# Kernel tuning notes

Hardware: AMD Instinct MI355X
Metric: run time of the kernel (lower is better)

## Reference

```python
import jax, jax.numpy as jnp
import numpy as np

EMBED_DIM = 768
HEAD_DIM = 64
BATCH = 8
SEQ = 4096


def setup_inputs() -> dict:
    key = jax.random.key(0)
    k_x, k_q, k_k, k_v = jax.random.split(key, 4)
    input_ids = jax.random.normal(k_x, (BATCH, SEQ, EMBED_DIM), dtype=jnp.float32)
    # nn.Linear(embed, head, bias=False): weight shape [head, embed]; y = x @ W.T
    scale = 1.0 / np.sqrt(EMBED_DIM)
    Wq = jax.random.normal(k_q, (HEAD_DIM, EMBED_DIM), dtype=jnp.float32) * scale
    Wk = jax.random.normal(k_k, (HEAD_DIM, EMBED_DIM), dtype=jnp.float32) * scale
    Wv = jax.random.normal(k_v, (HEAD_DIM, EMBED_DIM), dtype=jnp.float32) * scale
    return {"input_ids": input_ids, "Wq": Wq, "Wk": Wk, "Wv": Wv}


def reference(input_ids, Wq, Wk, Wv):
    # Projections. NOTE: the original module (faithfully reproduced) computes
    # v with q_net, so Wv is unused in the forward math.
    q = jnp.einsum('bse,he->bsh', input_ids, Wq)  # [B,S,H]
    k = jnp.einsum('bse,he->bsh', input_ids, Wk)  # [B,S,H]
    v = jnp.einsum('bse,he->bsh', input_ids, Wq)  # bug in source: uses q_net
    seq_len = q.shape[1]
    # Non-standard scaling: divide by sqrt(seq_len), not sqrt(head_dim)
    scores = jnp.einsum('bqh,bkh->bqk', q, k) / jnp.sqrt(jnp.float32(seq_len))
    # Non-standard softmax axis: over the query axis (dim=1)
    attn_weights = jax.nn.softmax(scores, axis=1)  # [B,Sq,Sk]
    return jnp.einsum('bqk,bkh->bqh', attn_weights, v)
```

## Files before the change

### kernel.cpp

```cpp
#include <hip/hip_runtime.h>
#include <hip/hip_bf16.h>
#include <cstdint>


#define BATCH 8
#define SEQ   4096
#define EMB   768
#define HD    64
#define NROW  (BATCH*SEQ)

#define QSCALE 0.1803368801111201f
#define KSCALE 0.125f
#define CSCALE 5.545177444479562f

typedef float  f32x4  __attribute__((ext_vector_type(4)));
typedef float  f32x16 __attribute__((ext_vector_type(16)));
typedef __bf16 bf16x8 __attribute__((ext_vector_type(8)));
typedef unsigned short u16x8_t __attribute__((ext_vector_type(8)));
typedef unsigned int   u32x4_t __attribute__((ext_vector_type(4)));

__device__ __forceinline__ f32x4 mfma16(bf16x8 a, bf16x8 b, f32x4 c) {
  return __builtin_amdgcn_mfma_f32_16x16x32_bf16(a, b, c, 0, 0, 0);
}
__device__ __forceinline__ f32x16 mfma32(bf16x8 a, bf16x8 b, f32x16 c) {
  return __builtin_amdgcn_mfma_f32_32x32x16_bf16(a, b, c, 0, 0, 0);
}
__device__ __forceinline__ unsigned short f2b(float f) {
  __bf16 h = (__bf16)f;
  return __builtin_bit_cast(unsigned short, h);
}
__device__ __forceinline__ float b2f(unsigned short u) {
  unsigned int x = ((unsigned int)u) << 16;
  return __builtin_bit_cast(float, x);
}
__device__ __forceinline__ unsigned short f2h(float f) {
  _Float16 h = (_Float16)f;
  return __builtin_bit_cast(unsigned short, h);
}
__device__ __forceinline__ float h2f(unsigned short u) {
  return (float)__builtin_bit_cast(_Float16, u);
}
__device__ __forceinline__ bf16x8 ldsA(const unsigned short* p) {
  return __builtin_bit_cast(bf16x8, *(const u16x8_t*)p);
}
__device__ __forceinline__ bf16x8 ldg8(const unsigned short* p) {
  return __builtin_bit_cast(bf16x8, *(const u16x8_t*)p);
}
__device__ __forceinline__ float expf2(float x) {
  float r; asm("v_exp_f32 %0, %1" : "=v"(r) : "v"(x)); return r;
}
__device__ __forceinline__ unsigned cvtpk(float lo, float hi) {
  unsigned r; asm("v_cvt_pk_bf16_f32 %0, %1, %2" : "=v"(r) : "v"(lo), "v"(hi)); return r;
}
__device__ __forceinline__ void plane32swap(unsigned &a, unsigned &b) {
  asm volatile("v_permlane32_swap_b32 %0, %1" : "+v"(a), "+v"(b));
}
__device__ __forceinline__ void glld16(const void* g, void* l) {
  __builtin_amdgcn_global_load_lds(
      (const __attribute__((address_space(1))) void*)g,
      (__attribute__((address_space(3))) void*)l, 16, 0, 0);
}
__device__ __forceinline__ int sidx(int r, int h) {
  return r * 64 + (h ^ ((r & 7) << 3));
}

__global__ __launch_bounds__(256) void wcvt_kernel(
    const float* __restrict__ Wq, const float* __restrict__ Wk,
    unsigned short* __restrict__ Wb) {
  int ci = blockIdx.x * 256 + threadIdx.x;
  int r = ci / 96, c8 = ci % 96;
  const float* src = (r < 64 ? Wq + (size_t)r * EMB : Wk + (size_t)(r - 64) * EMB) + c8 * 8;
  float4 a = *(const float4*)src, d = *(const float4*)(src + 4);
  u16x8_t o;
  o[0]=f2b(a.x); o[1]=f2b(a.y); o[2]=f2b(a.z); o[3]=f2b(a.w);
  o[4]=f2b(d.x); o[5]=f2b(d.y); o[6]=f2b(d.z); o[7]=f2b(d.w);
  *(u16x8_t*)(Wb + (size_t)ci * 8) = o;
}

__global__ __launch_bounds__(256) void proj_kernel(
    const float* __restrict__ X, const unsigned short* __restrict__ Wb,
    unsigned short* __restrict__ Qb, unsigned short* __restrict__ Kb) {
  __shared__ unsigned short Ws[2][8192];
  const int t = threadIdx.x, lane = t & 63, w = t >> 6;
  const int c = lane & 15, g = lane >> 4;
  const int row0 = blockIdx.x * 64;
  f32x4 acc[8];
#pragma unroll
  for (int f = 0; f < 8; ++f) { acc[f][0]=0.f; acc[f][1]=0.f; acc[f][2]=0.f; acc[f][3]=0.f; }

  auto STAGE = [&](int ec, int bb) {
#pragma unroll
    for (int i = 0; i < 4; ++i) {
      int rr = w + 4 * i;
      int ci = rr * 64 + lane;
      int r = ci >> 3, cL = ci & 7;
      glld16(Wb + (size_t)r * EMB + ec * 64 + (cL ^ (r & 7)) * 8, (void*)&Ws[bb][rr * 512]);
    }
  };
  const float* xrow = X + (size_t)(row0 + 16 * w + c) * EMB + 8 * g;
  float4 Xa[4], Xb[4];
  auto LOADX = [&](float4* R, int ec) {
    const float* xp = xrow + ec * 64;
    R[0] = *(const float4*)xp;        R[1] = *(const float4*)(xp + 4);
    R[2] = *(const float4*)(xp + 32); R[3] = *(const float4*)(xp + 36);
  };
  auto COMPUTE = [&](const float4* R, const unsigned short* Wt) {
    bf16x8 Af[2];
#pragma unroll
    for (int es = 0; es < 2; ++es) {
      float4 v0 = R[2 * es], v1 = R[2 * es + 1];
      u16x8_t tmp;
      tmp[0]=f2b(v0.x); tmp[1]=f2b(v0.y); tmp[2]=f2b(v0.z); tmp[3]=f2b(v0.w);
      tmp[4]=f2b(v1.x); tmp[5]=f2b(v1.y); tmp[6]=f2b(v1.z); tmp[7]=f2b(v1.w);
      Af[es] = __builtin_bit_cast(bf16x8, tmp);
    }
#pragma unroll
    for (int es = 0; es < 2; ++es)
#pragma unroll
      for (int f = 0; f < 8; ++f) {
        bf16x8 Bf = ldsA(&Wt[sidx(16 * f + c, es * 32 + 8 * g)]);
        acc[f] = mfma16(Af[es], Bf, acc[f]);
      }
  };

  LOADX(Xa, 0);
  STAGE(0, 0);
  __syncthreads();
#pragma unroll 1
  for (int e2 = 0; e2 < 6; ++e2) {
    int ec = 2 * e2;
    if (ec + 1 < 12) { STAGE(ec + 1, (ec + 1) & 1); LOADX(Xb, ec + 1); }
    COMPUTE(Xa, Ws[ec & 1]);
    __syncthreads();
    if (ec + 2 < 12) { STAGE(ec + 2, (ec + 2) & 1); LOADX(Xa, ec + 2); }
    COMPUTE(Xb, Ws[(ec + 1) & 1]);
    __syncthreads();
  }
#pragma unroll
  for (int f = 0; f < 8; ++f) {
    int n = 16 * f + c;
    float sc = (n < 64) ? QSCALE : KSCALE;
#pragma unroll
    for (int r = 0; r < 4; ++r) {
      int ROW = row0 + 16 * w + 4 * g + r;
      unsigned short bv = f2b(acc[f][r] * sc);
      if (n < 64) Qb[(size_t)ROW * 64 + n] = bv;
      else        Kb[(size_t)ROW * 64 + (n - 64)] = bv;
    }
  }
}

__global__ __launch_bounds__(256) void colsum_kernel(
    const unsigned short* __restrict__ Qb, const unsigned short* __restrict__ Kb,
    float* __restrict__ Zpart) {
  __shared__ unsigned short Qs[2][8192];
  const int t = threadIdx.x, lane = t & 63, w = t >> 6;
  const int c = lane & 31, hi = lane >> 5;
  const int fid = blockIdx.x;
  const int b = fid & 7, rem = fid >> 3;
  const int kt = rem & 15, qs = rem >> 4;
  const size_t kbase = (size_t)b * SEQ + kt * 256;
  const size_t qbase0 = (size_t)b * SEQ + qs * 1024;

  bf16x8 Kf[2][4];
#pragma unroll
  for (int j = 0; j < 2; ++j)
#pragma unroll
    for (int es = 0; es < 4; ++es)
      Kf[j][es] = __builtin_bit_cast(bf16x8,
          *(const u16x8_t*)(Kb + (kbase + 64 * w + 32 * j + c) * 64 + 16 * es + 8 * hi));

  const unsigned short* pq[4];
#pragma unroll
  for (int i = 0; i < 4; ++i) {
    int rr = w + 4 * i;
    int ci = rr * 64 + lane;
    int r = ci >> 3, cL = ci & 7;
    pq[i] = Qb + (qbase0 + r) * 64 + (cL ^ (r & 7)) * 8;
  }
  auto STAGE = [&](int bb) {
#pragma unroll
    for (int i = 0; i < 4; ++i) {
      glld16(pq[i], (void*)&Qs[bb][(w + 4 * i) * 512]);
      pq[i] += 8192;
    }
  };
  f32x16 fz16;
#pragma unroll
  for (int i = 0; i < 16; ++i) fz16[i] = 0.f;

  float csum[2] = {0.f, 0.f};
  STAGE(0);
  __syncthreads();
  for (int qi = 0; qi < 8; ++qi) {
    if (qi < 7) STAGE((qi + 1) & 1);
    const unsigned short* Qt = Qs[qi & 1];
#pragma unroll
    for (int sq = 0; sq < 4; ++sq) {
      bf16x8 A[4];
#pragma unroll
      for (int es = 0; es < 4; ++es)
        A[es] = ldsA(&Qt[sidx(32 * sq + c, 16 * es + 8 * hi)]);
#pragma unroll
      for (int j = 0; j < 2; ++j) {
        f32x16 sv = mfma32(A[0], Kf[j][0], fz16);
#pragma unroll
        for (int es = 1; es < 4; ++es) sv = mfma32(A[es], Kf[j][es], sv);
#pragma unroll
        for (int i = 0; i < 16; ++i) csum[j] += expf2(sv[i]);
      }
    }
    __syncthreads();
  }
#pragma unroll
  for (int j = 0; j < 2; ++j) {
    float v = csum[j] + __shfl_xor(csum[j], 32);
    if (lane < 32)
      Zpart[(kbase + 64 * w + 32 * j + lane) * 4 + qs] = v;
  }
}

__global__ __launch_bounds__(256) void vtrans_kernel(
    const unsigned short* __restrict__ Qb, const float* __restrict__ Zpart,
    unsigned short* __restrict__ VT) {
  __shared__ unsigned short T[128 * 72];
  __shared__ float cvs[128];
  const int t = threadIdx.x;
  const int kt = blockIdx.x, b = blockIdx.y;
  const size_t kbase = (size_t)b * SEQ + kt * 128;
#pragma unroll
  for (int it = 0; it < 4; ++it) {
    int ci = t + 256 * it;
    int r = ci >> 3, ch = ci & 7;
    u16x8_t v = *(const u16x8_t*)(Qb + (kbase + r) * 64 + 8 * ch);
    *(u16x8_t*)(&T[r * 72 + 8 * (ch ^ ((r >> 3) & 7))]) = v;
  }
  if (t < 128) {
    const float* zp = Zpart + (kbase + t) * 4;
    cvs[t] = CSCALE / (zp[0] + zp[1] + zp[2] + zp[3]);
  }
  __syncthreads();
#pragma unroll
  for (int it = 0; it < 4; ++it) {
    int ci = t + 256 * it;
    int h = ci >> 4, c16 = ci & 15;
    u16x8_t o;
#pragma unroll
    for (int j = 0; j < 8; ++j) {
      int r = 8 * c16 + j;
      unsigned short raw = T[r * 72 + 8 * ((h >> 3) ^ (c16 & 7)) + (h & 7)];
      o[j] = f2b(cvs[r] * b2f(raw));
    }
    *(u16x8_t*)(VT + ((size_t)(b * 64 + h)) * SEQ + kt * 128 + 8 * c16) = o;
  }
}

template <bool F16P>
__global__ __launch_bounds__(256) void attn_kernel(
    const unsigned short* __restrict__ Qb, const unsigned short* __restrict__ Kb,
    const unsigned short* __restrict__ VT, void* __restrict__ outp, int nkt) {
  __shared__ unsigned short KV[2][8192];
  const int t = threadIdx.x, lane = t & 63, w = t >> 6;
  const int c = lane & 31, hi = lane >> 5;
  const int fid = blockIdx.x;
  const int b = fid & 7, rem = fid >> 3;
  const int qt = rem & 15, ks = rem >> 4;
  const size_t brow = (size_t)b * SEQ;
  const int q0 = qt * 256;
  const int ntiles = 2 * nkt;
  const int t0 = ks * ntiles;

  bf16x8 Qf[2][4];
#pragma unroll
  for (int j = 0; j < 2; ++j)
#pragma unroll
    for (int es = 0; es < 4; ++es)
      Qf[j][es] = ldg8(Qb + (brow + q0 + 64 * w + 32 * j + c) * 64 + 16 * es + 8 * hi);

  f32x16 fz16;
#pragma unroll
  for (int i = 0; i < 16; ++i) fz16[i] = 0.f;

  f32x16 acc[2][2];
#pragma unroll
  for (int j = 0; j < 2; ++j)
#pragma unroll
    for (int hb = 0; hb < 2; ++hb)
#pragma unroll
      for (int i = 0; i < 16; ++i) acc[j][hb][i] = 0.f;

  const unsigned short *pk0, *pk1, *pv0, *pv1;
  {
    int ci0 = w * 64 + lane, ci1 = (w + 4) * 64 + lane;
    int r0 = ci0 >> 3, c0 = ci0 & 7, r1 = ci1 >> 3, c1 = ci1 & 7;
    pk0 = Kb + (brow + (size_t)t0 * 64 + r0) * 64 + (c0 ^ (r0 & 7)) * 8;
    pk1 = Kb + (brow + (size_t)t0 * 64 + r1) * 64 + (c1 ^ (r1 & 7)) * 8;
    int h0 = ci0 >> 3, h1 = ci1 >> 3;
    pv0 = VT + ((size_t)(b * 64 + h0)) * SEQ + t0 * 64 + (c0 ^ (h0 & 7)) * 8;
    pv1 = VT + ((size_t)(b * 64 + h1)) * SEQ + t0 * 64 + (c1 ^ (h1 & 7)) * 8;
  }
  auto STAGE = [&](int bb) {
    glld16(pk0, (void*)&KV[bb][w * 512]);
    glld16(pk1, (void*)&KV[bb][(w + 4) * 512]);
    glld16(pv0, (void*)&KV[bb][4096 + w * 512]);
    glld16(pv1, (void*)&KV[bb][4096 + (w + 4) * 512]);
    pk0 += 4096; pk1 += 4096; pv0 += 64; pv1 += 64;
  };

  auto COMPUTE = [&](int bb) {
    const unsigned short* Ks = &KV[bb][0];
    const unsigned short* Vs = &KV[bb][4096];
#pragma unroll
    for (int kb = 0; kb < 2; ++kb) {
      bf16x8 KA[4];
#pragma unroll
      for (int es = 0; es < 4; ++es)
        KA[es] = ldsA(&Ks[sidx(32 * kb + c, 16 * es + 8 * hi)]);
      bf16x8 fA[2][2];
#pragma unroll
      for (int j = 0; j < 2; ++j) {
        f32x16 sv = mfma32(KA[0], Qf[j][0], fz16);
#pragma unroll
        for (int es = 1; es < 4; ++es) sv = mfma32(KA[es], Qf[j][es], sv);
        float p[16];
#pragma unroll
        for (int i = 0; i < 16; ++i) p[i] = expf2(sv[i]);
        unsigned X0 = cvtpk(p[0], p[1]),  X1 = cvtpk(p[2], p[3]);
        unsigned Y0 = cvtpk(p[4], p[5]),  Y1 = cvtpk(p[6], p[7]);
        plane32swap(X0, Y0); plane32swap(X1, Y1);
        u32x4_t F0 = {X0, X1, Y0, Y1};
        unsigned Z0 = cvtpk(p[8], p[9]),   Z1 = cvtpk(p[10], p[11]);
        unsigned W0 = cvtpk(p[12], p[13]), W1 = cvtpk(p[14], p[15]);
        plane32swap(Z0, W0); plane32swap(Z1, W1);
        u32x4_t F1 = {Z0, Z1, W0, W1};
        fA[j][0] = __builtin_bit_cast(bf16x8, F0);
        fA[j][1] = __builtin_bit_cast(bf16x8, F1);
      }
#pragma unroll
      for (int hb = 0; hb < 2; ++hb) {
        int h = 32 * hb + c;
        int col0 = 32 * kb + 8 * hi;
        bf16x8 VB0 = ldsA(&Vs[h * 64 + (col0 ^ ((h & 7) << 3))]);
        bf16x8 VB1 = ldsA(&Vs[h * 64 + ((col0 + 16) ^ ((h & 7) << 3))]);
        acc[0][hb] = mfma32(fA[0][0], VB0, acc[0][hb]);
        acc[0][hb] = mfma32(fA[0][1], VB1, acc[0][hb]);
        acc[1][hb] = mfma32(fA[1][0], VB0, acc[1][hb]);
        acc[1][hb] = mfma32(fA[1][1], VB1, acc[1][hb]);
      }
    }
  };

  STAGE(0);
  __syncthreads();
  for (int tt = 0; tt < ntiles; ++tt) {
    if (tt + 1 < ntiles) STAGE((tt + 1) & 1);
    COMPUTE(tt & 1);
    __syncthreads();
  }
#pragma unroll
  for (int j = 0; j < 2; ++j)
#pragma unroll
    for (int hb = 0; hb < 2; ++hb)
#pragma unroll
      for (int r = 0; r < 16; ++r) {
        int qrow = (r & 3) + 8 * (r >> 2) + 4 * hi;
        size_t idx = (brow + q0 + 64 * w + 32 * j + qrow) * 64 + 32 * hb + c;
        if (F16P) {
          unsigned short* op = (unsigned short*)outp + (size_t)ks * NROW * 64;
          op[idx] = f2h(acc[j][hb][r]);
        } else {
          ((float*)outp)[idx] = acc[j][hb][r];
        }
      }
}

__global__ __launch_bounds__(256) void osum_kernel(
    const unsigned short* __restrict__ P, float* __restrict__ O) {
  const size_t PS = (size_t)NROW * 64;
  size_t i = ((size_t)blockIdx.x * 256 + threadIdx.x) * 8;
  u16x8_t a = *(const u16x8_t*)(P + i);
  u16x8_t b = *(const u16x8_t*)(P + PS + i);
  u16x8_t c = *(const u16x8_t*)(P + 2 * PS + i);
  u16x8_t d = *(const u16x8_t*)(P + 3 * PS + i);
  float o[8];
#pragma unroll
  for (int j = 0; j < 8; ++j)
    o[j] = (h2f(a[j]) + h2f(b[j])) + (h2f(c[j]) + h2f(d[j]));
  float4 o0 = {o[0], o[1], o[2], o[3]}, o1 = {o[4], o[5], o[6], o[7]};
  *(float4*)(O + i) = o0;
  *(float4*)(O + i + 4) = o1;
}

extern "C" void kernel_launch(void* const* d_in, const int* in_sizes, int n_in,
                              void* d_out, int out_size, void* d_ws, size_t ws_size,
                              hipStream_t stream) {
  const float* X  = (const float*)d_in[0];
  const float* Wq = (const float*)d_in[1];
  const float* Wk = (const float*)d_in[2];
  float* Out = (float*)d_out;

  unsigned char* wsb = (unsigned char*)d_ws;
  const size_t QB_OFF = 0;
  const size_t KB_OFF = 4194304;
  const size_t WB_OFF = 8388608;
  const size_t Z_OFF  = 8585216;
  const size_t VT_OFF = 9240576;
  const size_t OP_OFF = 13434880;
  const size_t TOTAL_SPLIT = OP_OFF + (size_t)4 * NROW * 64 * 2;

  unsigned short* Qb = (unsigned short*)(wsb + QB_OFF);
  unsigned short* Kb = (unsigned short*)(wsb + KB_OFF);
  unsigned short* Wb = (unsigned short*)(wsb + WB_OFF);
  float* Zpart       = (float*)(wsb + Z_OFF);
  unsigned short* VT = (unsigned short*)(wsb + VT_OFF);
  unsigned short* OpH = (unsigned short*)(wsb + OP_OFF);

  const bool split = (ws_size >= TOTAL_SPLIT);

  hipLaunchKernelGGL(wcvt_kernel, dim3(48), dim3(256), 0, stream, Wq, Wk, Wb);
  hipLaunchKernelGGL(proj_kernel, dim3(NROW / 64), dim3(256), 0, stream, X, Wb, Qb, Kb);
  hipLaunchKernelGGL(colsum_kernel, dim3(512), dim3(256), 0, stream, Qb, Kb, Zpart);
  hipLaunchKernelGGL(vtrans_kernel, dim3(32, 8), dim3(256), 0, stream, Qb, Zpart, VT);
  if (split) {
    hipLaunchKernelGGL(attn_kernel<true>, dim3(512), dim3(256), 0, stream,
                       Qb, Kb, VT, (void*)OpH, 8);
    hipLaunchKernelGGL(osum_kernel, dim3(1024), dim3(256), 0, stream, OpH, Out);
  } else {
    hipLaunchKernelGGL(attn_kernel<false>, dim3(128), dim3(256), 0, stream,
                       Qb, Kb, VT, (void*)Out, 32);
  }
}
```

Baseline: 101.2 us.

## Give each wave private K/V LDS tiles and replace barriers with vmcnt waits

The shared double-buffered K/V tile of 64 keys is replaced by per-wave double buffers holding 32 keys each. Every wave loads its own copy of K and V through global_load_lds and waits on vmcnt, so the block-wide __syncthreads barriers are gone. The goal is to stop waves from stalling on each other each iteration and to let them drift independently. In exchange, all four waves fetch the same K/V data, which roughly quadruples L2/global load traffic, and the tile loop runs twice as many shorter iterations.

```diff
diff --git a/kernel.cpp b/kernel.cpp
--- a/kernel.cpp
+++ b/kernel.cpp
@@ -59,6 +59,12 @@
   __builtin_amdgcn_global_load_lds(
       (const __attribute__((address_space(1))) void*)g,
       (__attribute__((address_space(3))) void*)l, 16, 0, 0);
+}
+__device__ __forceinline__ void vmwait8() {
+  asm volatile("s_waitcnt vmcnt(8)" ::: "memory");
+}
+__device__ __forceinline__ void vmwait0() {
+  asm volatile("s_waitcnt vmcnt(0)" ::: "memory");
 }
 __device__ __forceinline__ int sidx(int r, int h) {
   return r * 64 + (h ^ ((r & 7) << 3));
@@ -259,7 +265,7 @@
 __global__ __launch_bounds__(256) void attn_kernel(
     const unsigned short* __restrict__ Qb, const unsigned short* __restrict__ Kb,
     const unsigned short* __restrict__ VT, void* __restrict__ outp, int nkt) {
-  __shared__ unsigned short KV[2][8192];
+  __shared__ unsigned short KV[4][2][4096];
   const int t = threadIdx.x, lane = t & 63, w = t >> 6;
   const int c = lane & 31, hi = lane >> 5;
   const int fid = blockIdx.x;
@@ -267,8 +273,8 @@
   const int qt = rem & 15, ks = rem >> 4;
   const size_t brow = (size_t)b * SEQ;
   const int q0 = qt * 256;
-  const int ntiles = 2 * nkt;
-  const int t0 = ks * ntiles;
+  const int ntiles = 4 * nkt;
+  const int k00 = ks * ntiles * 32;
 
   bf16x8 Qf[2][4];
 #pragma unroll
@@ -289,73 +295,73 @@
 #pragma unroll
       for (int i = 0; i < 16; ++i) acc[j][hb][i] = 0.f;
 
-  const unsigned short *pk0, *pk1, *pv0, *pv1;
-  {
-    int ci0 = w * 64 + lane, ci1 = (w + 4) * 64 + lane;
-    int r0 = ci0 >> 3, c0 = ci0 & 7, r1 = ci1 >> 3, c1 = ci1 & 7;
-    pk0 = Kb + (brow + (size_t)t0 * 64 + r0) * 64 + (c0 ^ (r0 & 7)) * 8;
-    pk1 = Kb + (brow + (size_t)t0 * 64 + r1) * 64 + (c1 ^ (r1 & 7)) * 8;
-    int h0 = ci0 >> 3, h1 = ci1 >> 3;
-    pv0 = VT + ((size_t)(b * 64 + h0)) * SEQ + t0 * 64 + (c0 ^ (h0 & 7)) * 8;
-    pv1 = VT + ((size_t)(b * 64 + h1)) * SEQ + t0 * 64 + (c1 ^ (h1 & 7)) * 8;
-  }
+  const unsigned short* pkw =
+      Kb + (brow + (size_t)k00 + (lane >> 3)) * 64 +
+      8 * ((lane & 7) ^ ((lane >> 3) & 7));
+  const unsigned short* pvw =
+      VT + ((size_t)(b * 64 + (lane >> 2))) * SEQ + k00 +
+      8 * ((lane & 3) ^ ((lane >> 3) & 3));
+
   auto STAGE = [&](int bb) {
-    glld16(pk0, (void*)&KV[bb][w * 512]);
-    glld16(pk1, (void*)&KV[bb][(w + 4) * 512]);
-    glld16(pv0, (void*)&KV[bb][4096 + w * 512]);
-    glld16(pv1, (void*)&KV[bb][4096 + (w + 4) * 512]);
-    pk0 += 4096; pk1 += 4096; pv0 += 64; pv1 += 64;
-  };
+    unsigned short* base = &KV[w][bb][0];
+#pragma unroll
+    for (int i = 0; i < 4; ++i)
+      glld16(pkw + i * 512, (void*)(base + i * 512));
+#pragma unroll
+    for (int i = 0; i < 4; ++i)
+      glld16(pvw + (size_t)i * 16 * SEQ, (void*)(base + 2048 + i * 512));
+    pkw += 2048;
+    pvw += 32;
+  };
+
+  const int vsw = (c >> 1) & 3;
 
   auto COMPUTE = [&](int bb) {
-    const unsigned short* Ks = &KV[bb][0];
-    const unsigned short* Vs = &KV[bb][4096];
-#pragma unroll
-    for (int kb = 0; kb < 2; ++kb) {
-      bf16x8 KA[4];
-#pragma unroll
-      for (int es = 0; es < 4; ++es)
-        KA[es] = ldsA(&Ks[sidx(32 * kb + c, 16 * es + 8 * hi)]);
-      bf16x8 fA[2][2];
-#pragma unroll
-      for (int j = 0; j < 2; ++j) {
-        f32x16 sv = mfma32(KA[0], Qf[j][0], fz16);
-#pragma unroll
-        for (int es = 1; es < 4; ++es) sv = mfma32(KA[es], Qf[j][es], sv);
-        float p[16];
-#pragma unroll
-        for (int i = 0; i < 16; ++i) p[i] = expf2(sv[i]);
-        unsigned X0 = cvtpk(p[0], p[1]),  X1 = cvtpk(p[2], p[3]);
-        unsigned Y0 = cvtpk(p[4], p[5]),  Y1 = cvtpk(p[6], p[7]);
-        plane32swap(X0, Y0); plane32swap(X1, Y1);
-        u32x4_t F0 = {X0, X1, Y0, Y1};
-        unsigned Z0 = cvtpk(p[8], p[9]),   Z1 = cvtpk(p[10], p[11]);
-        unsigned W0 = cvtpk(p[12], p[13]), W1 = cvtpk(p[14], p[15]);
-        plane32swap(Z0, W0); plane32swap(Z1, W1);
-        u32x4_t F1 = {Z0, Z1, W0, W1};
-        fA[j][0] = __builtin_bit_cast(bf16x8, F0);
-        fA[j][1] = __builtin_bit_cast(bf16x8, F1);
-      }
-#pragma unroll
-      for (int hb = 0; hb < 2; ++hb) {
-        int h = 32 * hb + c;
-        int col0 = 32 * kb + 8 * hi;
-        bf16x8 VB0 = ldsA(&Vs[h * 64 + (col0 ^ ((h & 7) << 3))]);
-        bf16x8 VB1 = ldsA(&Vs[h * 64 + ((col0 + 16) ^ ((h & 7) << 3))]);
-        acc[0][hb] = mfma32(fA[0][0], VB0, acc[0][hb]);
-        acc[0][hb] = mfma32(fA[0][1], VB1, acc[0][hb]);
-        acc[1][hb] = mfma32(fA[1][0], VB0, acc[1][hb]);
-        acc[1][hb] = mfma32(fA[1][1], VB1, acc[1][hb]);
-      }
+    const unsigned short* Ks = &KV[w][bb][0];
+    const unsigned short* Vs = &KV[w][bb][2048];
+    bf16x8 KA[4];
+#pragma unroll
+    for (int es = 0; es < 4; ++es)
+      KA[es] = ldsA(&Ks[c * 64 + ((16 * es + 8 * hi) ^ ((c & 7) << 3))]);
+    bf16x8 fA[2][2];
+#pragma unroll
+    for (int j = 0; j < 2; ++j) {
+      f32x16 sv = mfma32(KA[0], Qf[j][0], fz16);
+#pragma unroll
+      for (int es = 1; es < 4; ++es) sv = mfma32(KA[es], Qf[j][es], sv);
+      float p[16];
+#pragma unroll
+      for (int i = 0; i < 16; ++i) p[i] = expf2(sv[i]);
+      unsigned X0 = cvtpk(p[0], p[1]),  X1 = cvtpk(p[2], p[3]);
+      unsigned Y0 = cvtpk(p[4], p[5]),  Y1 = cvtpk(p[6], p[7]);
+      plane32swap(X0, Y0); plane32swap(X1, Y1);
+      u32x4_t F0 = {X0, X1, Y0, Y1};
+      unsigned Z0 = cvtpk(p[8], p[9]),   Z1 = cvtpk(p[10], p[11]);
+      unsigned W0 = cvtpk(p[12], p[13]), W1 = cvtpk(p[14], p[15]);
+      plane32swap(Z0, W0); plane32swap(Z1, W1);
+      u32x4_t F1 = {Z0, Z1, W0, W1};
+      fA[j][0] = __builtin_bit_cast(bf16x8, F0);
+      fA[j][1] = __builtin_bit_cast(bf16x8, F1);
+    }
+#pragma unroll
+    for (int hb = 0; hb < 2; ++hb) {
+      int hrow = (32 * hb + c) * 32;
+      bf16x8 VB0 = ldsA(&Vs[hrow + 8 * (hi ^ vsw)]);
+      bf16x8 VB1 = ldsA(&Vs[hrow + 8 * ((2 + hi) ^ vsw)]);
+      acc[0][hb] = mfma32(fA[0][0], VB0, acc[0][hb]);
+      acc[0][hb] = mfma32(fA[0][1], VB1, acc[0][hb]);
+      acc[1][hb] = mfma32(fA[1][0], VB0, acc[1][hb]);
+      acc[1][hb] = mfma32(fA[1][1], VB1, acc[1][hb]);
     }
   };
 
   STAGE(0);
-  __syncthreads();
+#pragma unroll 1
   for (int tt = 0; tt < ntiles; ++tt) {
-    if (tt + 1 < ntiles) STAGE((tt + 1) & 1);
+    if (tt + 1 < ntiles) { STAGE((tt + 1) & 1); vmwait8(); }
+    else                 { vmwait0(); }
+    __builtin_amdgcn_sched_barrier(0);
     COMPUTE(tt & 1);
-    __syncthreads();
   }
 #pragma unroll
   for (int j = 0; j < 2; ++j)
```

Measured after the change: 109.4 us. +8.0%, slower.
